# Performance work log

Hardware: AMD Instinct MI355X
Metric: run time of the kernel (lower is better)

Reference implementation:

```python
import jax, jax.numpy as jnp
import numpy as np

B, T, E, H, V, C = 64, 1024, 256, 512, 30522, 2


def setup_inputs() -> dict:
    key = jax.random.key(0)
    ks = jax.random.split(key, 20)
    tokens = jax.random.randint(ks[0], (B, T), 0, V, dtype=jnp.int32)
    emb = jax.random.normal(ks[1], (V, E), dtype=jnp.float32) * 0.02
    def lin(k, out_d, in_d, bias_const=0.0):
        W = jax.random.normal(k, (out_d, in_d), dtype=jnp.float32) / np.sqrt(in_d)
        b = jnp.full((out_d,), bias_const, dtype=jnp.float32)
        return W, b
    # layer 0: input E, layer 1: input H
    Wr0, br0 = lin(ks[2], H, E + H)
    Wz0, bz0 = lin(ks[3], H, E + H, -2.0)
    Wh0, bh0 = lin(ks[4], H, E + H)
    Wr1, br1 = lin(ks[5], H, H + H)
    Wz1, bz1 = lin(ks[6], H, H + H, -2.0)
    Wh1, bh1 = lin(ks[7], H, H + H)
    fcW, fcb = lin(ks[8], C, H)
    return dict(tokens=tokens, emb=emb,
                Wr0=Wr0, br0=br0, Wz0=Wz0, bz0=bz0, Wh0=Wh0, bh0=bh0,
                Wr1=Wr1, br1=br1, Wz1=Wz1, bz1=bz1, Wh1=Wh1, bh1=bh1,
                fcW=fcW, fcb=fcb)


def _run_layer(xs, Wr, br, Wz, bz, Wh, bh):
    # xs: [B, T, D_in]. Weight layout [H, D_in + H] as torch Linear on cat([x, h]).
    D = xs.shape[-1]
    Wrx, Wrh = Wr[:, :D], Wr[:, D:]
    Wzx, Wzh = Wz[:, :D], Wz[:, D:]
    Whx, Whh = Wh[:, :D], Wh[:, D:]
    # Precompute input contributions for all timesteps (same math as per-step cat).
    xr = jnp.einsum('btd,hd->bth', xs, Wrx) + br
    xz = jnp.einsum('btd,hd->bth', xs, Wzx) + bz
    xh = jnp.einsum('btd,hd->bth', xs, Whx) + bh
    def step(h, inp):
        xr_t, xz_t, xh_t = inp
        r = jax.nn.sigmoid(xr_t + h @ Wrh.T)
        z = jax.nn.sigmoid(xz_t + h @ Wzh.T)
        h_tilde = jnp.tanh(xh_t + (r * h) @ Whh.T)
        h_new = (1.0 - z) * h + z * h_tilde
        return h_new, h_new
    h0 = jnp.zeros((xs.shape[0], Wr.shape[0]), dtype=xs.dtype)
    # time-major for scan
    seq = (xr.transpose(1, 0, 2), xz.transpose(1, 0, 2), xh.transpose(1, 0, 2))
    h_last, hs = jax.lax.scan(step, h0, seq)
    return hs.transpose(1, 0, 2), h_last  # [B,T,H], [B,H]


def reference(tokens, emb, Wr0, br0, Wz0, bz0, Wh0, bh0,
              Wr1, br1, Wz1, bz1, Wh1, bh1, fcW, fcb):
    x = emb[tokens]  # [B, T, E]
    hs0, _ = _run_layer(x, Wr0, br0, Wz0, bz0, Wh0, bh0)
    _, h_last = _run_layer(hs0, Wr1, br1, Wz1, bz1, Wh1, bh1)
    return h_last @ fcW.T + fcb  # [B, C]
```

## Files before the change

kernel.cpp:

```cpp
#include <hip/hip_runtime.h>
#include <math.h>

#define H0A_OFF  0
#define H0B_OFF  32768
#define H1_OFF   65536
#define RH0_OFF  98304
#define RH1_OFF  131072
#define FLG_OFF  163840
#define WS_FLOATS (163840 + 512)
#define WS_BYTES  (WS_FLOATS * 4)

#define SROW 516

__device__ __forceinline__ void gstore(float* p, float v) {
    __hip_atomic_store(p, v, __ATOMIC_RELAXED, __HIP_MEMORY_SCOPE_AGENT);
}
__device__ __forceinline__ unsigned gloadU(const unsigned* p) {
    return __hip_atomic_load(p, __ATOMIC_RELAXED, __HIP_MEMORY_SCOPE_AGENT);
}
__device__ __forceinline__ void gstoreU(unsigned* p, unsigned v) {
    __hip_atomic_store(p, v, __ATOMIC_RELAXED, __HIP_MEMORY_SCOPE_AGENT);
}
__device__ __forceinline__ float fma4(float4 w, float4 x, float a) {
    a = fmaf(w.x, x.x, a); a = fmaf(w.y, x.y, a);
    a = fmaf(w.z, x.z, a); a = fmaf(w.w, x.w, a);
    return a;
}

__device__ __forceinline__ void issue8(float4 t[8], const float* __restrict__ src, int tid) {
    #pragma unroll
    for (int i = 0; i < 8; ++i) {
        const float* p = src + 4 * tid + 2048 * i;
        asm volatile("global_load_dwordx4 %0, %1, off sc0 sc1"
                     : "=&v"(t[i]) : "v"(p) : "memory");
    }
}
__device__ __forceinline__ void drain_all() {
    asm volatile("s_waitcnt vmcnt(0)" ::: "memory");
}
__device__ __forceinline__ void drain_keep8() {
    asm volatile("s_waitcnt vmcnt(8)" ::: "memory");
}
__device__ __forceinline__ void lds_write8(float* __restrict__ buf, const float4 t[8], int tid) {
    #pragma unroll
    for (int i = 0; i < 8; ++i) {
        int f4i = tid + 512 * i;
        int row = f4i >> 7, col4 = f4i & 127;
        *(float4*)&buf[row * SROW + col4 * 4] = t[i];
    }
}

__device__ __forceinline__ void gbar(unsigned* arrD, unsigned* goOwn,
                                     const unsigned* goOth, int myIdx, bool agg,
                                     int tid, unsigned tag, unsigned otag) {
    __syncthreads();
    if (tid >= 512) {
        if (agg) {
            const int L = tid - 512;
            for (;;) {
                bool ok = ((int)(gloadU(arrD + L) - tag) >= 0) &&
                          ((int)(gloadU(goOth) - otag) >= 0);
                if (__ballot(ok) == ~0ull) break;
                __builtin_amdgcn_s_sleep(2);
            }
            if (tid == 512) gstoreU(goOwn, tag);
        }
    } else if (tid == 0) {
        gstoreU(arrD + myIdx, tag);
        while ((int)(gloadU(goOwn) - tag) < 0)
            __builtin_amdgcn_s_sleep(2);
    }
    __syncthreads();
}

__global__ __launch_bounds__(576, 1) void gru_main(
    const int* __restrict__ tokens, const float* __restrict__ emb,
    const float* __restrict__ Wr0, const float* __restrict__ br0,
    const float* __restrict__ Wz0, const float* __restrict__ bz0,
    const float* __restrict__ Wh0, const float* __restrict__ bh0,
    const float* __restrict__ Wr1, const float* __restrict__ br1,
    const float* __restrict__ Wz1, const float* __restrict__ bz1,
    const float* __restrict__ Wh1, const float* __restrict__ bh1,
    float* __restrict__ ws)
{
    const int blk = blockIdx.x;
    const int tid = threadIdx.x;
    const bool comp = tid < 512;

    const int rg    = (blk >> 2) & 1;
    const int jl    = blk & 3;
    const int jh    = (blk >> 3) & 15;
    const int layer = blk >> 7;
    const int j     = jh * 4 + jl;
    const int ks    = (tid >> 6) & 7;
    const int lane  = tid & 63;
    const int c     = lane >> 3;
    const int rgl   = lane & 7;
    const int rowbase = rg * 32;
    const int cg    = j * 8 + c;
    const int cR    = (tid >> 5) & 7;
    const int riR   = tid & 31;
    const int cgR   = j * 8 + cR;

    unsigned* flg  = (unsigned*)(ws + FLG_OFF);
    const int dom  = layer * 2 + rg;
    const int odom = (layer ? 0 : 2) + rg;
    unsigned* arrD  = flg + dom * 64;
    unsigned* goOwn = flg + 256 + dom * 16;
    unsigned* goOth = flg + 256 + odom * 16;
    const bool agg  = (j == 0);

    const int S1 = layer ? 512 : 256;
    const int K  = S1 + 512;
    const float* WrL = layer ? Wr1 : Wr0;
    const float* WzL = layer ? Wz1 : Wz0;
    const float* WhL = layer ? Wh1 : Wh0;
    const float* wrRow = WrL + (size_t)cg * K;
    const float* wzRow = WzL + (size_t)cg * K;
    const float* whRow = WhL + (size_t)cg * K;
    const float bR = (layer ? br1 : br0)[cgR];
    const float bZ = (layer ? bz1 : bz0)[cgR];
    const float bH = (layer ? bh1 : bh0)[cgR];

    const float* h0buf[2] = { ws + H0A_OFF, ws + H0B_OFF };
    float* h0bufW[2] = { ws + H0A_OFF, ws + H0B_OFF };
    float* h1p   = ws + H1_OFF;
    float* rhOwn = ws + (layer ? RH1_OFF : RH0_OFF);

    __shared__ float  bufA[32 * SROW];
    __shared__ float  pTmp[3 * 2048];
    __shared__ float4 wLDS[3072];

    if (comp) {
        const float* Wb[3] = {WrL, WzL, WhL};
        for (int idx = tid; idx < 3072; idx += 512) {
            int g = idx >> 10, rem = idx & 1023, chunk = rem >> 3, c8 = rem & 7;
            wLDS[(g * 128 + chunk) * 8 + c8] =
                *(const float4*)(Wb[g] + (size_t)(j * 8 + c8) * K + S1 + 4 * chunk);
        }
    }

    const int k1  = ks * (S1 >> 3);
    const int k2s = ks * 64;
    const int wch = ks * 16;

    for (int s = 0; s <= 1024; ++s) {
        const bool act = layer ? (s >= 1) : (s < 1024);
        float zv = 0.f, hp = 0.f, hx = 0.f;
        float aR[4] = {0,0,0,0}, aZ[4] = {0,0,0,0}, aH[4] = {0,0,0,0};
        float4 hpv[8];

        const float* hReadP  = layer ? (const float*)h1p : h0buf[(s - 1) & 1];
        float*       hWriteP = layer ? h1p : h0bufW[s & 1];
        const float* hInP    = h0buf[(s - 1) & 1];

        if (act && comp) {
            if (layer) {
                float4 t[8];
                issue8(t, hInP + rowbase * 512, tid);
                issue8(hpv, hReadP + rowbase * 512, tid);
                drain_keep8();
                lds_write8(bufA, t, tid);
            } else {
                float4 t[4];
                #pragma unroll
                for (int q = 0; q < 4; ++q) {
                    int f4i = tid + 512 * q;
                    int row = f4i >> 6, col4 = f4i & 63;
                    int tok = tokens[(rowbase + row) * 1024 + s];
                    t[q] = *(const float4*)(emb + (size_t)tok * 256 + col4 * 4);
                }
                issue8(hpv, hReadP + rowbase * 512, tid);
                drain_keep8();
                #pragma unroll
                for (int q = 0; q < 4; ++q) {
                    int f4i = tid + 512 * q;
                    int row = f4i >> 6, col4 = f4i & 63;
                    *(float4*)&bufA[row * SROW + col4 * 4] = t[q];
                }
            }
        }
        __syncthreads();

        if (act && comp) {
            const int nq1 = S1 >> 5;
            #pragma unroll 4
            for (int i = 0; i < nq1; ++i) {
                int kk = k1 + 4 * i;
                float4 w1 = *(const float4*)(wrRow + kk);
                float4 w2 = *(const float4*)(wzRow + kk);
                float4 w3 = *(const float4*)(whRow + kk);
                #pragma unroll
                for (int rr = 0; rr < 4; ++rr) {
                    float4 xv = *(const float4*)(&bufA[(rgl + 8 * rr) * SROW + kk]);
                    aR[rr] = fma4(w1, xv, aR[rr]);
                    aZ[rr] = fma4(w2, xv, aZ[rr]);
                    aH[rr] = fma4(w3, xv, aH[rr]);
                }
            }
        }
        __syncthreads();

        if (act && comp) {
            drain_all();
            lds_write8(bufA, hpv, tid);
        }
        __syncthreads();

        if (act && comp) {
            #pragma unroll 4
            for (int i = 0; i < 16; ++i) {
                int kst = k2s + 4 * i;
                float4 w1 = wLDS[(wch + i) * 8 + c];
                float4 w2 = wLDS[(128 + wch + i) * 8 + c];
                #pragma unroll
                for (int rr = 0; rr < 4; ++rr) {
                    float4 xv = *(const float4*)(&bufA[(rgl + 8 * rr) * SROW + kst]);
                    aR[rr] = fma4(w1, xv, aR[rr]);
                    aZ[rr] = fma4(w2, xv, aZ[rr]);
                }
            }
            #pragma unroll
            for (int rr = 0; rr < 4; ++rr) {
                int o = ks * 256 + c * 32 + (rgl + 8 * rr);
                pTmp[o]        = aR[rr];
                pTmp[2048 + o] = aZ[rr];
                pTmp[4096 + o] = aH[rr];
            }
        }
        __syncthreads();

        if (act && tid < 256) {
            int o = cR * 32 + riR;
            float sR = 0.f, sZ = 0.f, sH = 0.f;
            #pragma unroll
            for (int p = 0; p < 8; ++p) {
                sR += pTmp[o + 256 * p];
                sZ += pTmp[2048 + o + 256 * p];
                sH += pTmp[4096 + o + 256 * p];
            }
            float rv = 1.f / (1.f + expf(-(sR + bR)));
            zv = 1.f / (1.f + expf(-(sZ + bZ)));
            hx = sH;
            hp = bufA[riR * SROW + cgR];
            gstore(rhOwn + (rowbase + riR) * 512 + cgR, rv * hp);
        }

        gbar(arrD, goOwn, goOth, j, agg, tid, (unsigned)(2 * s + 1),
             (!layer && s >= 2) ? (unsigned)(2 * s - 1) : 0u);

        if (act && comp) {
            float4 t[8];
            issue8(t, rhOwn + rowbase * 512, tid);
            drain_all();
            lds_write8(bufA, t, tid);
        }
        __syncthreads();

        if (act && comp) {
            float a[4] = {0,0,0,0};
            #pragma unroll 4
            for (int i = 0; i < 16; ++i) {
                int kst = k2s + 4 * i;
                float4 w3 = wLDS[(256 + wch + i) * 8 + c];
                #pragma unroll
                for (int rr = 0; rr < 4; ++rr) {
                    float4 xv = *(const float4*)(&bufA[(rgl + 8 * rr) * SROW + kst]);
                    a[rr] = fma4(w3, xv, a[rr]);
                }
            }
            #pragma unroll
            for (int rr = 0; rr < 4; ++rr)
                pTmp[ks * 256 + c * 32 + (rgl + 8 * rr)] = a[rr];
        }
        __syncthreads();

        if (act && tid < 256) {
            int o = cR * 32 + riR;
            float sH2 = 0.f;
            #pragma unroll
            for (int p = 0; p < 8; ++p) sH2 += pTmp[o + 256 * p];
            float ht = tanhf(hx + sH2 + bH);
            float hn = (1.f - zv) * hp + zv * ht;
            gstore(hWriteP + (rowbase + riR) * 512 + cgR, hn);
        }

        gbar(arrD, goOwn, goOth, j, agg, tid, (unsigned)(2 * s + 2),
             layer ? (unsigned)(2 * s + 2) : 0u);
    }
}

__global__ __launch_bounds__(128) void gru_fc(
    const float* __restrict__ h1f, const float* __restrict__ fcW,
    const float* __restrict__ fcb, float* __restrict__ out)
{
    int tid = threadIdx.x;
    int b = tid >> 1, cc = tid & 1;
    const float* hrow = h1f + b * 512;
    const float* wrow = fcW + cc * 512;
    float acc = 0.f;
    #pragma unroll 4
    for (int k = 0; k < 512; k += 4) {
        float4 hv = *(const float4*)(hrow + k);
        float4 wv = *(const float4*)(wrow + k);
        acc = fmaf(hv.x, wv.x, fmaf(hv.y, wv.y, fmaf(hv.z, wv.z, fmaf(hv.w, wv.w, acc))));
    }
    out[b * 2 + cc] = acc + fcb[cc];
}

extern "C" void kernel_launch(void* const* d_in, const int* in_sizes, int n_in,
                              void* d_out, int out_size, void* d_ws, size_t ws_size,
                              hipStream_t stream) {
    const int* tokens = (const int*)d_in[0];
    const float* emb = (const float*)d_in[1];
    const float* Wr0 = (const float*)d_in[2];  const float* br0 = (const float*)d_in[3];
    const float* Wz0 = (const float*)d_in[4];  const float* bz0 = (const float*)d_in[5];
    const float* Wh0 = (const float*)d_in[6];  const float* bh0 = (const float*)d_in[7];
    const float* Wr1 = (const float*)d_in[8];  const float* br1 = (const float*)d_in[9];
    const float* Wz1 = (const float*)d_in[10]; const float* bz1 = (const float*)d_in[11];
    const float* Wh1 = (const float*)d_in[12]; const float* bh1 = (const float*)d_in[13];
    const float* fcW = (const float*)d_in[14]; const float* fcb = (const float*)d_in[15];
    float* ws = (float*)d_ws;

    hipMemsetAsync(d_ws, 0, WS_BYTES, stream);

    gru_main<<<256, 576, 0, stream>>>(tokens, emb, Wr0, br0, Wz0, bz0, Wh0, bh0,
                                      Wr1, br1, Wz1, bz1, Wh1, bh1, ws);
    gru_fc<<<1, 128, 0, stream>>>(ws + H1_OFF, fcW, fcb, (float*)d_out);
}
```

Measured before the change: 18.33 ms.

## Widen GRU blocks to 1024 threads, splitting batch rows across two wave groups

Each block now runs 16 waves instead of 8 compute waves plus a barrier-polling wave. Each wave handles half of the 32 batch rows, so per-thread loads, LDS writes and FMA work per step are halved. Barrier polling moves onto wave 0 of the aggregator block instead of a dedicated extra wave. The aim is shorter per-timestep latency on the serial recurrence, at the cost of weight rows being loaded twice per block and extra pressure on LDS and registers.

```diff
diff --git a/kernel.cpp b/kernel.cpp
--- a/kernel.cpp
+++ b/kernel.cpp
@@ -27,10 +27,10 @@
     return a;
 }
 
-__device__ __forceinline__ void issue8(float4 t[8], const float* __restrict__ src, int tid) {
+__device__ __forceinline__ void issue4(float4 t[4], const float* __restrict__ src, int tid) {
     #pragma unroll
-    for (int i = 0; i < 8; ++i) {
-        const float* p = src + 4 * tid + 2048 * i;
+    for (int i = 0; i < 4; ++i) {
+        const float* p = src + 4 * tid + 4096 * i;
         asm volatile("global_load_dwordx4 %0, %1, off sc0 sc1"
                      : "=&v"(t[i]) : "v"(p) : "memory");
     }
@@ -38,13 +38,13 @@
 __device__ __forceinline__ void drain_all() {
     asm volatile("s_waitcnt vmcnt(0)" ::: "memory");
 }
-__device__ __forceinline__ void drain_keep8() {
-    asm volatile("s_waitcnt vmcnt(8)" ::: "memory");
-}
-__device__ __forceinline__ void lds_write8(float* __restrict__ buf, const float4 t[8], int tid) {
+__device__ __forceinline__ void drain_keep4() {
+    asm volatile("s_waitcnt vmcnt(4)" ::: "memory");
+}
+__device__ __forceinline__ void lds_write4(float* __restrict__ buf, const float4 t[4], int tid) {
     #pragma unroll
-    for (int i = 0; i < 8; ++i) {
-        int f4i = tid + 512 * i;
+    for (int i = 0; i < 4; ++i) {
+        int f4i = tid + 1024 * i;
         int row = f4i >> 7, col4 = f4i & 127;
         *(float4*)&buf[row * SROW + col4 * 4] = t[i];
     }
@@ -54,16 +54,16 @@
                                      const unsigned* goOth, int myIdx, bool agg,
                                      int tid, unsigned tag, unsigned otag) {
     __syncthreads();
-    if (tid >= 512) {
-        if (agg) {
-            const int L = tid - 512;
+    if (agg) {
+        if (tid < 64) {
+            if (tid == 0) gstoreU(arrD + myIdx, tag);
             for (;;) {
-                bool ok = ((int)(gloadU(arrD + L) - tag) >= 0) &&
+                bool ok = ((int)(gloadU(arrD + tid) - tag) >= 0) &&
                           ((int)(gloadU(goOth) - otag) >= 0);
                 if (__ballot(ok) == ~0ull) break;
                 __builtin_amdgcn_s_sleep(2);
             }
-            if (tid == 512) gstoreU(goOwn, tag);
+            if (tid == 0) gstoreU(goOwn, tag);
         }
     } else if (tid == 0) {
         gstoreU(arrD + myIdx, tag);
@@ -73,7 +73,7 @@
     __syncthreads();
 }
 
-__global__ __launch_bounds__(576, 1) void gru_main(
+__global__ __launch_bounds__(1024, 1) void gru_main(
     const int* __restrict__ tokens, const float* __restrict__ emb,
     const float* __restrict__ Wr0, const float* __restrict__ br0,
     const float* __restrict__ Wz0, const float* __restrict__ bz0,
@@ -85,14 +85,15 @@
 {
     const int blk = blockIdx.x;
     const int tid = threadIdx.x;
-    const bool comp = tid < 512;
 
     const int rg    = (blk >> 2) & 1;
     const int jl    = blk & 3;
     const int jh    = (blk >> 3) & 15;
     const int layer = blk >> 7;
     const int j     = jh * 4 + jl;
-    const int ks    = (tid >> 6) & 7;
+    const int wave  = tid >> 6;
+    const int ks    = wave & 7;
+    const int rrh   = (wave >> 3) & 1;
     const int lane  = tid & 63;
     const int c     = lane >> 3;
     const int rgl   = lane & 7;
@@ -131,9 +132,9 @@
     __shared__ float  pTmp[3 * 2048];
     __shared__ float4 wLDS[3072];
 
-    if (comp) {
+    {
         const float* Wb[3] = {WrL, WzL, WhL};
-        for (int idx = tid; idx < 3072; idx += 512) {
+        for (int idx = tid; idx < 3072; idx += 1024) {
             int g = idx >> 10, rem = idx & 1023, chunk = rem >> 3, c8 = rem & 7;
             wLDS[(g * 128 + chunk) * 8 + c8] =
                 *(const float4*)(Wb[g] + (size_t)(j * 8 + c8) * K + S1 + 4 * chunk);
@@ -143,38 +144,38 @@
     const int k1  = ks * (S1 >> 3);
     const int k2s = ks * 64;
     const int wch = ks * 16;
+    const int nq1 = S1 >> 5;
 
     for (int s = 0; s <= 1024; ++s) {
         const bool act = layer ? (s >= 1) : (s < 1024);
         float zv = 0.f, hp = 0.f, hx = 0.f;
-        float aR[4] = {0,0,0,0}, aZ[4] = {0,0,0,0}, aH[4] = {0,0,0,0};
-        float4 hpv[8];
-
-        const float* hReadP  = layer ? (const float*)h1p : h0buf[(s - 1) & 1];
-        float*       hWriteP = layer ? h1p : h0bufW[s & 1];
-        const float* hInP    = h0buf[(s - 1) & 1];
-
-        if (act && comp) {
+        float aR[2] = {0,0}, aZ[2] = {0,0}, aH[2] = {0,0};
+        float4 hpv[4];
+
+        const float* hReadP = layer ? (const float*)h1p : h0buf[(s - 1) & 1];
+        const float* hInP   = h0buf[(s - 1) & 1];
+
+        if (act) {
             if (layer) {
-                float4 t[8];
-                issue8(t, hInP + rowbase * 512, tid);
-                issue8(hpv, hReadP + rowbase * 512, tid);
-                drain_keep8();
-                lds_write8(bufA, t, tid);
+                float4 t[4];
+                issue4(t, hInP + rowbase * 512, tid);
+                issue4(hpv, hReadP + rowbase * 512, tid);
+                drain_keep4();
+                lds_write4(bufA, t, tid);
             } else {
-                float4 t[4];
-                #pragma unroll
-                for (int q = 0; q < 4; ++q) {
-                    int f4i = tid + 512 * q;
+                float4 t[2];
+                #pragma unroll
+                for (int q = 0; q < 2; ++q) {
+                    int f4i = tid + 1024 * q;
                     int row = f4i >> 6, col4 = f4i & 63;
                     int tok = tokens[(rowbase + row) * 1024 + s];
                     t[q] = *(const float4*)(emb + (size_t)tok * 256 + col4 * 4);
                 }
-                issue8(hpv, hReadP + rowbase * 512, tid);
-                drain_keep8();
-                #pragma unroll
-                for (int q = 0; q < 4; ++q) {
-                    int f4i = tid + 512 * q;
+                issue4(hpv, hReadP + rowbase * 512, tid);
+                drain_keep4();
+                #pragma unroll
+                for (int q = 0; q < 2; ++q) {
+                    int f4i = tid + 1024 * q;
                     int row = f4i >> 6, col4 = f4i & 63;
                     *(float4*)&bufA[row * SROW + col4 * 4] = t[q];
                 }
@@ -182,8 +183,7 @@
         }
         __syncthreads();
 
-        if (act && comp) {
-            const int nq1 = S1 >> 5;
+        if (act) {
             #pragma unroll 4
             for (int i = 0; i < nq1; ++i) {
                 int kk = k1 + 4 * i;
@@ -191,41 +191,43 @@
                 float4 w2 = *(const float4*)(wzRow + kk);
                 float4 w3 = *(const float4*)(whRow + kk);
                 #pragma unroll
-                for (int rr = 0; rr < 4; ++rr) {
+                for (int q = 0; q < 2; ++q) {
+                    int rr = 2 * rrh + q;
                     float4 xv = *(const float4*)(&bufA[(rgl + 8 * rr) * SROW + kk]);
-                    aR[rr] = fma4(w1, xv, aR[rr]);
-                    aZ[rr] = fma4(w2, xv, aZ[rr]);
-                    aH[rr] = fma4(w3, xv, aH[rr]);
-                }
-            }
-        }
-        __syncthreads();
-
-        if (act && comp) {
+                    aR[q] = fma4(w1, xv, aR[q]);
+                    aZ[q] = fma4(w2, xv, aZ[q]);
+                    aH[q] = fma4(w3, xv, aH[q]);
+                }
+            }
+        }
+        __syncthreads();
+
+        if (act) {
             drain_all();
-            lds_write8(bufA, hpv, tid);
-        }
-        __syncthreads();
-
-        if (act && comp) {
+            lds_write4(bufA, hpv, tid);
+        }
+        __syncthreads();
+
+        if (act) {
             #pragma unroll 4
             for (int i = 0; i < 16; ++i) {
                 int kst = k2s + 4 * i;
                 float4 w1 = wLDS[(wch + i) * 8 + c];
                 float4 w2 = wLDS[(128 + wch + i) * 8 + c];
                 #pragma unroll
-                for (int rr = 0; rr < 4; ++rr) {
+                for (int q = 0; q < 2; ++q) {
+                    int rr = 2 * rrh + q;
                     float4 xv = *(const float4*)(&bufA[(rgl + 8 * rr) * SROW + kst]);
-                    aR[rr] = fma4(w1, xv, aR[rr]);
-                    aZ[rr] = fma4(w2, xv, aZ[rr]);
+                    aR[q] = fma4(w1, xv, aR[q]);
+                    aZ[q] = fma4(w2, xv, aZ[q]);
                 }
             }
             #pragma unroll
-            for (int rr = 0; rr < 4; ++rr) {
-                int o = ks * 256 + c * 32 + (rgl + 8 * rr);
-                pTmp[o]        = aR[rr];
-                pTmp[2048 + o] = aZ[rr];
-                pTmp[4096 + o] = aH[rr];
+            for (int q = 0; q < 2; ++q) {
+                int o = ks * 256 + c * 32 + (rgl + 8 * (2 * rrh + q));
+                pTmp[o]        = aR[q];
+                pTmp[2048 + o] = aZ[q];
+                pTmp[4096 + o] = aH[q];
             }
         }
         __syncthreads();
@@ -249,33 +251,35 @@
         gbar(arrD, goOwn, goOth, j, agg, tid, (unsigned)(2 * s + 1),
              (!layer && s >= 2) ? (unsigned)(2 * s - 1) : 0u);
 
-        if (act && comp) {
-            float4 t[8];
-            issue8(t, rhOwn + rowbase * 512, tid);
+        if (act) {
+            float4 trh[4];
+            issue4(trh, rhOwn + rowbase * 512, tid);
             drain_all();
-            lds_write8(bufA, t, tid);
-        }
-        __syncthreads();
-
-        if (act && comp) {
-            float a[4] = {0,0,0,0};
+            lds_write4(bufA, trh, tid);
+        }
+        __syncthreads();
+
+        if (act) {
+            float a3[2] = {0,0};
             #pragma unroll 4
             for (int i = 0; i < 16; ++i) {
                 int kst = k2s + 4 * i;
                 float4 w3 = wLDS[(256 + wch + i) * 8 + c];
                 #pragma unroll
-                for (int rr = 0; rr < 4; ++rr) {
+                for (int q = 0; q < 2; ++q) {
+                    int rr = 2 * rrh + q;
                     float4 xv = *(const float4*)(&bufA[(rgl + 8 * rr) * SROW + kst]);
-                    a[rr] = fma4(w3, xv, a[rr]);
+                    a3[q] = fma4(w3, xv, a3[q]);
                 }
             }
             #pragma unroll
-            for (int rr = 0; rr < 4; ++rr)
-                pTmp[ks * 256 + c * 32 + (rgl + 8 * rr)] = a[rr];
+            for (int q = 0; q < 2; ++q)
+                pTmp[ks * 256 + c * 32 + (rgl + 8 * (2 * rrh + q))] = a3[q];
         }
         __syncthreads();
 
         if (act && tid < 256) {
+            float* hWriteP = layer ? h1p : h0bufW[s & 1];
             int o = cR * 32 + riR;
             float sH2 = 0.f;
             #pragma unroll
@@ -324,7 +328,7 @@
 
     hipMemsetAsync(d_ws, 0, WS_BYTES, stream);
 
-    gru_main<<<256, 576, 0, stream>>>(tokens, emb, Wr0, br0, Wz0, bz0, Wh0, bh0,
-                                      Wr1, br1, Wz1, bz1, Wh1, bh1, ws);
+    gru_main<<<256, 1024, 0, stream>>>(tokens, emb, Wr0, br0, Wz0, bz0, Wh0, bh0,
+                                       Wr1, br1, Wz1, bz1, Wh1, bh1, ws);
     gru_fc<<<1, 128, 0, stream>>>(ws + H1_OFF, fcW, fcb, (float*)d_out);
 }
```

Result: slower. 19.06 ms (+4.0%).

## Give each wave its own K-slice to drop intra-block barriers and helper wave

Applied to the files above, without the earlier changes.

Each wave now loads and writes only the K-slice of the hidden/input tiles it later reads, so the __syncthreads between staging and compute are removed within each phase. The dedicated 64-thread aggregator wave is removed: wave 0 of the aggregator block both arrives and polls. Recurrent weights are no longer cached in LDS and are read from global memory each step, while a second LDS buffer holds the h tile. This cuts block-level barriers per timestep but adds global weight traffic and makes the aggregator's arrival share a wave with polling.

```diff
diff --git a/kernel.cpp b/kernel.cpp
--- a/kernel.cpp
+++ b/kernel.cpp
@@ -27,43 +27,45 @@
     return a;
 }
 
-__device__ __forceinline__ void issue8(float4 t[8], const float* __restrict__ src, int tid) {
+__device__ __forceinline__ void issueSlice(float4 t[8], const float* __restrict__ src,
+                                           int lane, int cbase) {
     #pragma unroll
     for (int i = 0; i < 8; ++i) {
-        const float* p = src + 4 * tid + 2048 * i;
+        int f4i = lane + 64 * i, rowL = f4i >> 4, c4 = f4i & 15;
+        const float* p = src + rowL * 512 + cbase + 4 * c4;
         asm volatile("global_load_dwordx4 %0, %1, off sc0 sc1"
                      : "=&v"(t[i]) : "v"(p) : "memory");
     }
 }
+__device__ __forceinline__ void writeSlice(float* __restrict__ buf, const float4 t[8],
+                                           int lane, int cbase) {
+    #pragma unroll
+    for (int i = 0; i < 8; ++i) {
+        int f4i = lane + 64 * i, rowL = f4i >> 4, c4 = f4i & 15;
+        *(float4*)&buf[rowL * SROW + cbase + 4 * c4] = t[i];
+    }
+}
 __device__ __forceinline__ void drain_all() {
     asm volatile("s_waitcnt vmcnt(0)" ::: "memory");
 }
 __device__ __forceinline__ void drain_keep8() {
     asm volatile("s_waitcnt vmcnt(8)" ::: "memory");
-}
-__device__ __forceinline__ void lds_write8(float* __restrict__ buf, const float4 t[8], int tid) {
-    #pragma unroll
-    for (int i = 0; i < 8; ++i) {
-        int f4i = tid + 512 * i;
-        int row = f4i >> 7, col4 = f4i & 127;
-        *(float4*)&buf[row * SROW + col4 * 4] = t[i];
-    }
 }
 
 __device__ __forceinline__ void gbar(unsigned* arrD, unsigned* goOwn,
                                      const unsigned* goOth, int myIdx, bool agg,
                                      int tid, unsigned tag, unsigned otag) {
     __syncthreads();
-    if (tid >= 512) {
-        if (agg) {
-            const int L = tid - 512;
+    if (agg) {
+        if (tid < 64) {
+            if (tid == 0) gstoreU(arrD + myIdx, tag);
             for (;;) {
-                bool ok = ((int)(gloadU(arrD + L) - tag) >= 0) &&
+                bool ok = ((int)(gloadU(arrD + tid) - tag) >= 0) &&
                           ((int)(gloadU(goOth) - otag) >= 0);
                 if (__ballot(ok) == ~0ull) break;
                 __builtin_amdgcn_s_sleep(2);
             }
-            if (tid == 512) gstoreU(goOwn, tag);
+            if (tid == 0) gstoreU(goOwn, tag);
         }
     } else if (tid == 0) {
         gstoreU(arrD + myIdx, tag);
@@ -73,7 +75,7 @@
     __syncthreads();
 }
 
-__global__ __launch_bounds__(576, 1) void gru_main(
+__global__ __launch_bounds__(512, 1) void gru_main(
     const int* __restrict__ tokens, const float* __restrict__ emb,
     const float* __restrict__ Wr0, const float* __restrict__ br0,
     const float* __restrict__ Wz0, const float* __restrict__ bz0,
@@ -85,14 +87,13 @@
 {
     const int blk = blockIdx.x;
     const int tid = threadIdx.x;
-    const bool comp = tid < 512;
 
     const int rg    = (blk >> 2) & 1;
     const int jl    = blk & 3;
     const int jh    = (blk >> 3) & 15;
     const int layer = blk >> 7;
     const int j     = jh * 4 + jl;
-    const int ks    = (tid >> 6) & 7;
+    const int ks    = tid >> 6;
     const int lane  = tid & 63;
     const int c     = lane >> 3;
     const int rgl   = lane & 7;
@@ -127,63 +128,46 @@
     float* h1p   = ws + H1_OFF;
     float* rhOwn = ws + (layer ? RH1_OFF : RH0_OFF);
 
-    __shared__ float  bufA[32 * SROW];
-    __shared__ float  pTmp[3 * 2048];
-    __shared__ float4 wLDS[3072];
-
-    if (comp) {
-        const float* Wb[3] = {WrL, WzL, WhL};
-        for (int idx = tid; idx < 3072; idx += 512) {
-            int g = idx >> 10, rem = idx & 1023, chunk = rem >> 3, c8 = rem & 7;
-            wLDS[(g * 128 + chunk) * 8 + c8] =
-                *(const float4*)(Wb[g] + (size_t)(j * 8 + c8) * K + S1 + 4 * chunk);
-        }
-    }
-
-    const int k1  = ks * (S1 >> 3);
-    const int k2s = ks * 64;
-    const int wch = ks * 16;
+    __shared__ float bufA[32 * SROW];
+    __shared__ float bufB[32 * SROW];
+    __shared__ float pTmp[3 * 2048];
+
+    const int k1     = ks * (S1 >> 3);
+    const int k2s    = ks * 64;
+    const int k2base = S1 + k2s;
+    const int nq1    = S1 >> 5;
 
     for (int s = 0; s <= 1024; ++s) {
         const bool act = layer ? (s >= 1) : (s < 1024);
         float zv = 0.f, hp = 0.f, hx = 0.f;
         float aR[4] = {0,0,0,0}, aZ[4] = {0,0,0,0}, aH[4] = {0,0,0,0};
-        float4 hpv[8];
-
-        const float* hReadP  = layer ? (const float*)h1p : h0buf[(s - 1) & 1];
-        float*       hWriteP = layer ? h1p : h0bufW[s & 1];
-        const float* hInP    = h0buf[(s - 1) & 1];
-
-        if (act && comp) {
+
+        if (act) {
+            const float* hReadP = layer ? (const float*)h1p : h0buf[(s - 1) & 1];
+            float4 thp[8];
             if (layer) {
-                float4 t[8];
-                issue8(t, hInP + rowbase * 512, tid);
-                issue8(hpv, hReadP + rowbase * 512, tid);
+                float4 tx[8];
+                issueSlice(tx, h0buf[(s - 1) & 1] + rowbase * 512, lane, k1);
+                issueSlice(thp, hReadP + rowbase * 512, lane, k2s);
                 drain_keep8();
-                lds_write8(bufA, t, tid);
+                writeSlice(bufA, tx, lane, k1);
             } else {
-                float4 t[4];
-                #pragma unroll
-                for (int q = 0; q < 4; ++q) {
-                    int f4i = tid + 512 * q;
-                    int row = f4i >> 6, col4 = f4i & 63;
-                    int tok = tokens[(rowbase + row) * 1024 + s];
-                    t[q] = *(const float4*)(emb + (size_t)tok * 256 + col4 * 4);
-                }
-                issue8(hpv, hReadP + rowbase * 512, tid);
+                float4 tx[4];
+                #pragma unroll
+                for (int i = 0; i < 4; ++i) {
+                    int f4i = lane + 64 * i, rowL = f4i >> 3, c4 = f4i & 7;
+                    int tok = tokens[(rowbase + rowL) * 1024 + s];
+                    tx[i] = *(const float4*)(emb + (size_t)tok * 256 + k1 + 4 * c4);
+                }
+                issueSlice(thp, hReadP + rowbase * 512, lane, k2s);
                 drain_keep8();
                 #pragma unroll
-                for (int q = 0; q < 4; ++q) {
-                    int f4i = tid + 512 * q;
-                    int row = f4i >> 6, col4 = f4i & 63;
-                    *(float4*)&bufA[row * SROW + col4 * 4] = t[q];
-                }
-            }
-        }
-        __syncthreads();
-
-        if (act && comp) {
-            const int nq1 = S1 >> 5;
+                for (int i = 0; i < 4; ++i) {
+                    int f4i = lane + 64 * i, rowL = f4i >> 3, c4 = f4i & 7;
+                    *(float4*)&bufA[rowL * SROW + k1 + 4 * c4] = tx[i];
+                }
+            }
+
             #pragma unroll 4
             for (int i = 0; i < nq1; ++i) {
                 int kk = k1 + 4 * i;
@@ -198,24 +182,19 @@
                     aH[rr] = fma4(w3, xv, aH[rr]);
                 }
             }
-        }
-        __syncthreads();
-
-        if (act && comp) {
+
             drain_all();
-            lds_write8(bufA, hpv, tid);
-        }
-        __syncthreads();
-
-        if (act && comp) {
+            writeSlice(bufB, thp, lane, k2s);
+
             #pragma unroll 4
             for (int i = 0; i < 16; ++i) {
+                int kw  = k2base + 4 * i;
                 int kst = k2s + 4 * i;
-                float4 w1 = wLDS[(wch + i) * 8 + c];
-                float4 w2 = wLDS[(128 + wch + i) * 8 + c];
+                float4 w1 = *(const float4*)(wrRow + kw);
+                float4 w2 = *(const float4*)(wzRow + kw);
                 #pragma unroll
                 for (int rr = 0; rr < 4; ++rr) {
-                    float4 xv = *(const float4*)(&bufA[(rgl + 8 * rr) * SROW + kst]);
+                    float4 xv = *(const float4*)(&bufB[(rgl + 8 * rr) * SROW + kst]);
                     aR[rr] = fma4(w1, xv, aR[rr]);
                     aZ[rr] = fma4(w2, xv, aZ[rr]);
                 }
@@ -242,40 +221,38 @@
             float rv = 1.f / (1.f + expf(-(sR + bR)));
             zv = 1.f / (1.f + expf(-(sZ + bZ)));
             hx = sH;
-            hp = bufA[riR * SROW + cgR];
+            hp = bufB[riR * SROW + cgR];
             gstore(rhOwn + (rowbase + riR) * 512 + cgR, rv * hp);
         }
 
         gbar(arrD, goOwn, goOth, j, agg, tid, (unsigned)(2 * s + 1),
              (!layer && s >= 2) ? (unsigned)(2 * s - 1) : 0u);
 
-        if (act && comp) {
-            float4 t[8];
-            issue8(t, rhOwn + rowbase * 512, tid);
+        if (act) {
+            float4 trh[8];
+            issueSlice(trh, rhOwn + rowbase * 512, lane, k2s);
             drain_all();
-            lds_write8(bufA, t, tid);
-        }
-        __syncthreads();
-
-        if (act && comp) {
-            float a[4] = {0,0,0,0};
+            writeSlice(bufB, trh, lane, k2s);
+            float a3[4] = {0,0,0,0};
             #pragma unroll 4
             for (int i = 0; i < 16; ++i) {
+                int kw  = k2base + 4 * i;
                 int kst = k2s + 4 * i;
-                float4 w3 = wLDS[(256 + wch + i) * 8 + c];
+                float4 w3 = *(const float4*)(whRow + kw);
                 #pragma unroll
                 for (int rr = 0; rr < 4; ++rr) {
-                    float4 xv = *(const float4*)(&bufA[(rgl + 8 * rr) * SROW + kst]);
-                    a[rr] = fma4(w3, xv, a[rr]);
+                    float4 xv = *(const float4*)(&bufB[(rgl + 8 * rr) * SROW + kst]);
+                    a3[rr] = fma4(w3, xv, a3[rr]);
                 }
             }
             #pragma unroll
             for (int rr = 0; rr < 4; ++rr)
-                pTmp[ks * 256 + c * 32 + (rgl + 8 * rr)] = a[rr];
+                pTmp[ks * 256 + c * 32 + (rgl + 8 * rr)] = a3[rr];
         }
         __syncthreads();
 
         if (act && tid < 256) {
+            float* hWriteP = layer ? h1p : h0bufW[s & 1];
             int o = cR * 32 + riR;
             float sH2 = 0.f;
             #pragma unroll
@@ -324,7 +301,7 @@
 
     hipMemsetAsync(d_ws, 0, WS_BYTES, stream);
 
-    gru_main<<<256, 576, 0, stream>>>(tokens, emb, Wr0, br0, Wz0, bz0, Wh0, bh0,
+    gru_main<<<256, 512, 0, stream>>>(tokens, emb, Wr0, br0, Wz0, bz0, Wh0, bh0,
                                       Wr1, br1, Wz1, bz1, Wh1, bh1, ws);
     gru_fc<<<1, 128, 0, stream>>>(ws + H1_OFF, fcW, fcb, (float*)d_out);
 }
```

New measurement: 14.72 ms. 19.7% less time.
